# Performance work log

Hardware: AMD Instinct MI355X
Metric: run time of the kernel (lower is better)

The kernel has to match this reference:

```python
import jax, jax.numpy as jnp
import numpy as np
import math

FEAT_DIM = 256
QUERY_DIM = 256
HIDDEN = 64
OUT_DIM = 256
HEADS = 8


def setup_inputs() -> dict:
    key = jax.random.key(0)
    ks = jax.random.split(key, 10)
    B, NQ, NKV = 2, 2048, 2048
    s_q = 1.0 / math.sqrt(QUERY_DIM)
    s_f = 1.0 / math.sqrt(FEAT_DIM)
    s_o = 1.0 / math.sqrt(HIDDEN * HEADS)
    return {
        "feat": jax.random.normal(ks[0], (B, NKV, FEAT_DIM), jnp.float32),
        "query": jax.random.normal(ks[1], (B, NQ, QUERY_DIM), jnp.float32),
        # stacked per-head weights (each head has its own Linear in torch)
        "Wq": jax.random.uniform(ks[2], (HEADS, QUERY_DIM, HIDDEN), jnp.float32, -s_q, s_q),
        "bq": jax.random.uniform(ks[3], (HEADS, HIDDEN), jnp.float32, -s_q, s_q),
        "Wk": jax.random.uniform(ks[4], (HEADS, FEAT_DIM, HIDDEN), jnp.float32, -s_f, s_f),
        "bk": jax.random.uniform(ks[5], (HEADS, HIDDEN), jnp.float32, -s_f, s_f),
        "Wv": jax.random.uniform(ks[6], (HEADS, FEAT_DIM, HIDDEN), jnp.float32, -s_f, s_f),
        "bv": jax.random.uniform(ks[7], (HEADS, HIDDEN), jnp.float32, -s_f, s_f),
        "Wo": jax.random.uniform(ks[8], (HEADS * HIDDEN, OUT_DIM), jnp.float32, -s_o, s_o),
        "bo": jax.random.uniform(ks[9], (OUT_DIM,), jnp.float32, -s_o, s_o),
    }


def reference(feat, query, Wq, bq, Wk, bk, Wv, bv, Wo, bo):
    # Per-head projections, vectorized over the head axis h.
    # q: [B, H, Nq, E]; k, v: [B, H, Nkv, E]
    q = jnp.einsum("bnd,hde->bhne", query, Wq) + bq[None, :, None, :]
    k = jnp.einsum("bnd,hde->bhne", feat, Wk) + bk[None, :, None, :]
    v = jnp.einsum("bnd,hde->bhne", feat, Wv) + bv[None, :, None, :]
    scale = 1.0 / math.sqrt(HIDDEN)
    scores = jnp.einsum("bhqe,bhke->bhqk", q, k) * scale  # [B, H, Nq, Nkv]
    prob = jax.nn.softmax(scores, axis=-1)
    # dropout p=0.0 (eval) -> identity
    heads = jnp.einsum("bhqk,bhke->bhqe", prob, v)  # [B, H, Nq, E]
    # concat heads in order (head 0 first) then output projection
    B, H, NQ, E = heads.shape
    cat = heads.transpose(0, 2, 1, 3).reshape(B, NQ, H * E)
    return cat @ Wo + bo
```

## Files before the change

kernel.cpp:

```cpp
#include <hip/hip_runtime.h>
#include <hip/hip_bf16.h>

typedef unsigned short u16;
typedef __attribute__((ext_vector_type(8))) short short8;
typedef __attribute__((ext_vector_type(4))) float f32x4;
typedef __attribute__((ext_vector_type(16))) float f32x16;
typedef __attribute__((ext_vector_type(2))) int v2i;

#define HEADS 8
#define HID 64
#define QSCALE 0.18033688011112042f

__device__ inline u16 f2bf(float f){
    unsigned u = __float_as_uint(f);
    unsigned r = (u + 0x7fffu + ((u >> 16) & 1u)) >> 16;
    return (u16)r;
}

__device__ inline int cvtpk(float lo, float hi){
    int r;
    asm("v_cvt_pk_bf16_f32 %0, %1, %2" : "=v"(r) : "v"(lo), "v"(hi));
    return r;
}

__device__ inline float exp2fast(float x){
    float r;
    asm("v_exp_f32 %0, %1" : "=v"(r) : "v"(x));
    return r;
}

__device__ inline float xhalf_sum(float x){
    v2i r = __builtin_amdgcn_permlane32_swap(__float_as_int(x), __float_as_int(x), false, false);
    return __int_as_float(r.x) + __int_as_float(r.y);
}

__global__ __launch_bounds__(256) void prep_weights(
    const float* __restrict__ query, const float* __restrict__ feat,
    const float* __restrict__ Wq, const float* __restrict__ Wk,
    const float* __restrict__ Wv, const float* __restrict__ Wo,
    u16* __restrict__ Xbq, u16* __restrict__ Xbf,
    u16* __restrict__ WqT, u16* __restrict__ WkT, u16* __restrict__ WvT,
    u16* __restrict__ WoT)
{
    int id = blockIdx.x * 256 + threadIdx.x;
    if (id < 262144) {
        const float* src = (id < 131072) ? query : feat;
        u16* dst = (id < 131072) ? Xbq : Xbf;
        int r = (id < 131072) ? id : id - 131072;
        float4 a = *reinterpret_cast<const float4*>(&src[r * 8]);
        float4 b = *reinterpret_cast<const float4*>(&src[r * 8 + 4]);
        uint4 s;
        s.x = (unsigned)cvtpk(a.x, a.y);
        s.y = (unsigned)cvtpk(a.z, a.w);
        s.z = (unsigned)cvtpk(b.x, b.y);
        s.w = (unsigned)cvtpk(b.z, b.w);
        *reinterpret_cast<uint4*>(&dst[r * 8]) = s;
    } else if (id < 655360) {
        int id2 = id - 262144;
        int w = id2 / 131072;
        int r = id2 % 131072;
        int c = r >> 8;
        int d = r & 255;
        const float* W = (w == 0) ? Wq : (w == 1 ? Wk : Wv);
        u16* WT = (w == 0) ? WqT : (w == 1 ? WkT : WvT);
        WT[c * 256 + d] = f2bf(W[(c >> 6) * (256 * 64) + d * 64 + (c & 63)]);
    } else {
        int r = id - 655360;
        int o = r >> 9;
        int k = r & 511;
        WoT[o * 512 + k] = f2bf(Wo[k * 256 + o]);
    }
}

__global__ __launch_bounds__(256) void proj_kernel(
    const u16* __restrict__ Xbq, const u16* __restrict__ Xbf,
    const u16* __restrict__ WqT, const u16* __restrict__ WkT, const u16* __restrict__ WvT,
    const float* __restrict__ bq, const float* __restrict__ bk, const float* __restrict__ bv,
    u16* __restrict__ Qb, u16* __restrict__ KVf)
{
    int lb = blockIdx.x;
    int t8 = lb & 7;
    int m = lb >> 3;
    int which = (m < 64) ? 0 : (m < 128 ? 1 : 2);
    int mm = m & 63;
    int m0 = (((t8 >> 2) << 5) | (mm & 31)) * 64;
    int n0 = (((t8 & 3) << 1) | (mm >> 5)) * 64;

    const u16* Xb = (which == 0) ? Xbq : Xbf;
    const u16* WT = (which == 0) ? WqT : (which == 1 ? WkT : WvT);
    const float* bias = (which == 0) ? bq : (which == 1 ? bk : bv);
    int t = threadIdx.x;
    int lane = t & 63, w = t >> 6;
    int l15 = lane & 15, kof = (lane >> 4) * 8;

    __shared__ __align__(16) u16 lA[64][72];
    __shared__ __align__(16) u16 lB[64][72];

    f32x4 acc[4] = {};
    for (int kt = 0; kt < 256; kt += 64) {
        #pragma unroll
        for (int i = 0; i < 2; i++) {
            int lin = t + i * 256;
            int row = lin >> 3, c8 = (lin & 7) * 8;
            *reinterpret_cast<uint4*>(&lA[row][c8]) =
                *reinterpret_cast<const uint4*>(&Xb[(m0 + row) * 256 + kt + c8]);
            *reinterpret_cast<uint4*>(&lB[row][c8]) =
                *reinterpret_cast<const uint4*>(&WT[(n0 + row) * 256 + kt + c8]);
        }
        __syncthreads();
        #pragma unroll
        for (int ks = 0; ks < 2; ks++) {
            short8 a = *reinterpret_cast<const short8*>(&lA[w * 16 + l15][ks * 32 + kof]);
            #pragma unroll
            for (int nt = 0; nt < 4; nt++) {
                short8 b = *reinterpret_cast<const short8*>(&lB[nt * 16 + l15][ks * 32 + kof]);
                acc[nt] = __builtin_amdgcn_mfma_f32_16x16x32_bf16(a, b, acc[nt], 0, 0, 0);
            }
        }
        __syncthreads();
    }
    #pragma unroll
    for (int nt = 0; nt < 4; nt++) {
        #pragma unroll
        for (int i = 0; i < 4; i++) {
            int mrow = m0 + w * 16 + (lane >> 4) * 4 + i;
            int col = n0 + nt * 16 + l15;
            float val = acc[nt][i] + bias[col];
            int b_ = mrow >> 11, n = mrow & 2047;
            int h = col >> 6, e = col & 63;
            int bh = b_ * 8 + h;
            if (which == 0) {
                Qb[(bh * 2048 + n) * 64 + e] = f2bf(val * QSCALE);
            } else {
                int tile = n >> 6, nl = n & 63;
                size_t base = ((size_t)(bh * 32 + tile)) * 8192;
                size_t idx;
                if (which == 1) {
                    int reg  = ((nl >> 5) << 2) | (e >> 4);
                    int ln   = (nl & 31) | (((e >> 3) & 1) << 5);
                    idx = base + reg * 512 + ln * 8 + (e & 7);
                } else {
                    int reg  = ((e >> 5) << 2) | (nl >> 4);
                    int ln   = (e & 31) | (((nl >> 3) & 1) << 5);
                    idx = base + 4096 + reg * 512 + ln * 8 + (nl & 7);
                }
                KVf[idx] = f2bf(val);
            }
        }
    }
}

__global__ __launch_bounds__(512, 2) void attn_kernel(
    const u16* __restrict__ Qb, const u16* __restrict__ KVf, u16* __restrict__ cat)
{
    int lb = blockIdx.x;
    int chunk = lb >> 4;
    int bh = ((lb & 7) << 1) | ((lb >> 3) & 1);
    int b_ = bh >> 3, head = bh & 7;
    int t = threadIdx.x, lane = t & 63, w = t >> 6;
    int l31 = lane & 31, hh = lane >> 5;
    int sp = w >> 1, kvh = w & 1, wi = w >> 1;
    int q0 = chunk * 128 + sp * 32;

    __shared__ __align__(16) u16 smem[34304];
    u16* tiles = smem;
    float* Ol = (float*)smem;
    float* Ll = (float*)((char*)smem + 67584);

    const u16* KVfB = KVf + ((size_t)(bh * 32 + kvh * 16)) * 8192;

    short8 qf[4];
    {
        const u16* qp = Qb + (bh * 2048 + q0 + l31) * 64 + hh * 8;
        #pragma unroll
        for (int kc = 0; kc < 4; kc++)
            qf[kc] = *reinterpret_cast<const short8*>(qp + kc * 16);
    }
    asm volatile("s_waitcnt vmcnt(0)" ::: "memory");

#define PACKP(sb, base, out) {                                              \
        int A0 = cvtpk(sb[base+0], sb[base+1]);                             \
        int B0 = cvtpk(sb[base+4], sb[base+5]);                             \
        v2i r0 = __builtin_amdgcn_permlane32_swap(A0, B0, false, false);    \
        int A1 = cvtpk(sb[base+2], sb[base+3]);                             \
        int B1 = cvtpk(sb[base+6], sb[base+7]);                             \
        v2i r1 = __builtin_amdgcn_permlane32_swap(A1, B1, false, false);    \
        union { int i[4]; short8 s; } uu;                                   \
        uu.i[0] = r0.x; uu.i[1] = r1.x; uu.i[2] = r0.y; uu.i[3] = r1.y;     \
        out = uu.s; }

    auto stage = [&](int buf, int tile) {
        const u16* gsrc = KVfB + (size_t)tile * 8192;
        u16* ldst = tiles + (kvh * 2 + buf) * 8192;
        #pragma unroll
        for (int c = 0; c < 4; c++) {
            int off = (wi * 4 + c) * 512 + lane * 8;
            __builtin_amdgcn_global_load_lds(
                (const __attribute__((address_space(1))) unsigned int*)(const void*)(gsrc + off),
                (__attribute__((address_space(3))) unsigned int*)(void*)(ldst + off),
                16, 0, 0);
        }
    };

    f32x16 o0 = {}, o1 = {};
    float ac0 = 0.f, ac1 = 0.f, ac2 = 0.f, ac3 = 0.f;

    stage(0, 0);
    int cur = 0;
    for (int tt = 0; tt < 16; tt++) {
        if (tt < 15) {
            stage(cur ^ 1, tt + 1);
            asm volatile("s_waitcnt vmcnt(4)" ::: "memory");
        } else {
            asm volatile("s_waitcnt vmcnt(0)" ::: "memory");
        }
        __builtin_amdgcn_s_barrier();
        __builtin_amdgcn_sched_barrier(0);

        const u16* kbase = tiles + (kvh * 2 + cur) * 8192;
        short8 kf[8], vf[8];
        #pragma unroll
        for (int r = 0; r < 8; r++)
            kf[r] = *reinterpret_cast<const short8*>(kbase + r * 512 + lane * 8);
        #pragma unroll
        for (int r = 0; r < 8; r++)
            vf[r] = *reinterpret_cast<const short8*>(kbase + 4096 + r * 512 + lane * 8);

        f32x16 s0 = {}, s1 = {};
        #pragma unroll
        for (int kc = 0; kc < 4; kc++)
            s0 = __builtin_amdgcn_mfma_f32_32x32x16_bf16(kf[kc], qf[kc], s0, 0, 0, 0);
        #pragma unroll
        for (int kc = 0; kc < 4; kc++)
            s1 = __builtin_amdgcn_mfma_f32_32x32x16_bf16(kf[4 + kc], qf[kc], s1, 0, 0, 0);

        #pragma unroll
        for (int r = 0; r < 16; r++) {
            float p0 = exp2fast(s0[r]);
            float p1 = exp2fast(s1[r]);
            s0[r] = p0; s1[r] = p1;
            if ((r & 3) == 0) ac0 += p0 + p1;
            else if ((r & 3) == 1) ac1 += p0 + p1;
            else if ((r & 3) == 2) ac2 += p0 + p1;
            else ac3 += p0 + p1;
        }

        short8 pf[4];
        PACKP(s0, 0, pf[0]); PACKP(s0, 8, pf[1]);
        PACKP(s1, 0, pf[2]); PACKP(s1, 8, pf[3]);

        #pragma unroll
        for (int c = 0; c < 4; c++) {
            o0 = __builtin_amdgcn_mfma_f32_32x32x16_bf16(vf[c],     pf[c], o0, 0, 0, 0);
            o1 = __builtin_amdgcn_mfma_f32_32x32x16_bf16(vf[4 + c], pf[c], o1, 0, 0, 0);
        }

        asm volatile("s_waitcnt lgkmcnt(0)" ::: "memory");
        __builtin_amdgcn_s_barrier();
        __builtin_amdgcn_sched_barrier(0);
        cur ^= 1;
    }

    float lrun = xhalf_sum((ac0 + ac1) + (ac2 + ac3));

    #pragma unroll
    for (int eb = 0; eb < 2; eb++) {
        #pragma unroll
        for (int r = 0; r < 16; r++) {
            int d = eb * 32 + (r & 3) + 8 * (r >> 2) + 4 * hh;
            Ol[(w * 64 + d) * 33 + l31] = eb ? o1[r] : o0[r];
        }
    }
    if (hh == 0) Ll[w * 32 + l31] = lrun;
    __syncthreads();

    {
        int msp = t >> 7;
        int tt2 = t & 127;
        int q = tt2 >> 2;
        int d0 = (tt2 & 3) * 16;
        int wA = msp * 2, wB = msp * 2 + 1;
        float lsum = Ll[wA * 32 + q] + Ll[wB * 32 + q];
        float linv = 1.0f / lsum;
        float vv[16];
        #pragma unroll
        for (int j = 0; j < 16; j++)
            vv[j] = (Ol[(wA * 64 + d0 + j) * 33 + q] +
                     Ol[(wB * 64 + d0 + j) * 33 + q]) * linv;
        uint4 st0, st1;
        st0.x = (unsigned)cvtpk(vv[0],  vv[1]);
        st0.y = (unsigned)cvtpk(vv[2],  vv[3]);
        st0.z = (unsigned)cvtpk(vv[4],  vv[5]);
        st0.w = (unsigned)cvtpk(vv[6],  vv[7]);
        st1.x = (unsigned)cvtpk(vv[8],  vv[9]);
        st1.y = (unsigned)cvtpk(vv[10], vv[11]);
        st1.z = (unsigned)cvtpk(vv[12], vv[13]);
        st1.w = (unsigned)cvtpk(vv[14], vv[15]);
        u16* crow = cat + (b_ * 2048 + chunk * 128 + msp * 32 + q) * 512 + head * 64 + d0;
        *reinterpret_cast<uint4*>(crow) = st0;
        *reinterpret_cast<uint4*>(crow + 8) = st1;
    }
#undef PACKP
}

__global__ __launch_bounds__(256) void outproj_kernel(
    const u16* __restrict__ cat, const u16* __restrict__ WoT,
    const float* __restrict__ bo, float* __restrict__ out)
{
    int m0 = blockIdx.x * 64, n0 = blockIdx.y * 64;
    int t = threadIdx.x, lane = t & 63, w = t >> 6;
    int l15 = lane & 15, kof = (lane >> 4) * 8;

    __shared__ __align__(16) u16 lA[64][72];
    __shared__ __align__(16) u16 lB[64][72];

    f32x4 acc[4] = {};
    for (int kt = 0; kt < 512; kt += 64) {
        #pragma unroll
        for (int i = 0; i < 2; i++) {
            int lin = t + i * 256;
            int row = lin >> 3, c8 = (lin & 7) * 8;
            *reinterpret_cast<uint4*>(&lA[row][c8]) =
                *reinterpret_cast<const uint4*>(&cat[(m0 + row) * 512 + kt + c8]);
            *reinterpret_cast<uint4*>(&lB[row][c8]) =
                *reinterpret_cast<const uint4*>(&WoT[(n0 + row) * 512 + kt + c8]);
        }
        __syncthreads();
        #pragma unroll
        for (int ks = 0; ks < 2; ks++) {
            short8 a = *reinterpret_cast<const short8*>(&lA[w * 16 + l15][ks * 32 + kof]);
            #pragma unroll
            for (int nt = 0; nt < 4; nt++) {
                short8 b = *reinterpret_cast<const short8*>(&lB[nt * 16 + l15][ks * 32 + kof]);
                acc[nt] = __builtin_amdgcn_mfma_f32_16x16x32_bf16(a, b, acc[nt], 0, 0, 0);
            }
        }
        __syncthreads();
    }
    #pragma unroll
    for (int i = 0; i < 4; i++) {
        int mrow = m0 + w * 16 + (lane >> 4) * 4 + i;
        #pragma unroll
        for (int nt = 0; nt < 4; nt++) {
            int col = n0 + nt * 16 + l15;
            out[mrow * 256 + col] = acc[nt][i] + bo[col];
        }
    }
}

extern "C" void kernel_launch(void* const* d_in, const int* in_sizes, int n_in,
                              void* d_out, int out_size, void* d_ws, size_t ws_size,
                              hipStream_t stream) {
    const float* feat  = (const float*)d_in[0];
    const float* query = (const float*)d_in[1];
    const float* Wq = (const float*)d_in[2];
    const float* bq = (const float*)d_in[3];
    const float* Wk = (const float*)d_in[4];
    const float* bk = (const float*)d_in[5];
    const float* Wv = (const float*)d_in[6];
    const float* bv = (const float*)d_in[7];
    const float* Wo = (const float*)d_in[8];
    const float* bo = (const float*)d_in[9];
    float* out = (float*)d_out;

    char* ws = (char*)d_ws;
    u16* WqT = (u16*)(ws + 0);
    u16* WkT = (u16*)(ws + 262144);
    u16* WvT = (u16*)(ws + 524288);
    u16* WoT = (u16*)(ws + 786432);
    u16* Qb  = (u16*)(ws + 1048576);
    u16* KVf = (u16*)(ws + 5242880);
    u16* cat = (u16*)(ws + 13631488);
    u16* Xbq = (u16*)(ws + 17825792);
    u16* Xbf = (u16*)(ws + 19922944);

    hipLaunchKernelGGL(prep_weights, dim3(3072), dim3(256), 0, stream,
                       query, feat, Wq, Wk, Wv, Wo, Xbq, Xbf, WqT, WkT, WvT, WoT);
    hipLaunchKernelGGL(proj_kernel, dim3(1536), dim3(256), 0, stream,
                       Xbq, Xbf, WqT, WkT, WvT, bq, bk, bv, Qb, KVf);
    hipLaunchKernelGGL(attn_kernel, dim3(256), dim3(512), 0, stream,
                       Qb, KVf, cat);
    hipLaunchKernelGGL(outproj_kernel, dim3(64, 4), dim3(256), 0, stream,
                       cat, WoT, bo, out);
}
```

Measured before the change: 52.51 us.

## Pre-swizzle projection operands into MFMA fragment layout and use 32x32 MFMA

After: 51.22 us (median of 2 runs). -2.5%, faster.

```diff
diff --git a/kernel.cpp b/kernel.cpp
--- a/kernel.cpp
+++ b/kernel.cpp
@@ -39,14 +39,16 @@
     const float* __restrict__ Wq, const float* __restrict__ Wk,
     const float* __restrict__ Wv, const float* __restrict__ Wo,
     u16* __restrict__ Xbq, u16* __restrict__ Xbf,
-    u16* __restrict__ WqT, u16* __restrict__ WkT, u16* __restrict__ WvT,
-    u16* __restrict__ WoT)
+    u16* __restrict__ WfT, u16* __restrict__ WoT)
 {
     int id = blockIdx.x * 256 + threadIdx.x;
     if (id < 262144) {
         const float* src = (id < 131072) ? query : feat;
         u16* dst = (id < 131072) ? Xbq : Xbf;
         int r = (id < 131072) ? id : id - 131072;
+        int row = r >> 5;
+        int rb = row >> 5, r5 = row & 31;
+        int ks = (r & 31) >> 1, hi = r & 1;
         float4 a = *reinterpret_cast<const float4*>(&src[r * 8]);
         float4 b = *reinterpret_cast<const float4*>(&src[r * 8 + 4]);
         uint4 s;
@@ -54,7 +56,7 @@
         s.y = (unsigned)cvtpk(a.z, a.w);
         s.z = (unsigned)cvtpk(b.x, b.y);
         s.w = (unsigned)cvtpk(b.z, b.w);
-        *reinterpret_cast<uint4*>(&dst[r * 8]) = s;
+        *reinterpret_cast<uint4*>(&dst[((rb * 16 + ks) * 64 + hi * 32 + r5) * 8]) = s;
     } else if (id < 655360) {
         int id2 = id - 262144;
         int w = id2 / 131072;
@@ -62,8 +64,9 @@
         int c = r >> 8;
         int d = r & 255;
         const float* W = (w == 0) ? Wq : (w == 1 ? Wk : Wv);
-        u16* WT = (w == 0) ? WqT : (w == 1 ? WkT : WvT);
-        WT[c * 256 + d] = f2bf(W[(c >> 6) * (256 * 64) + d * 64 + (c & 63)]);
+        size_t idx = (size_t)(((w * 16 + (c >> 5)) * 16 + (d >> 4)) * 64
+                              + ((d >> 3) & 1) * 32 + (c & 31)) * 8 + (d & 7);
+        WfT[idx] = f2bf(W[(c >> 6) * (256 * 64) + d * 64 + (c & 63)]);
     } else {
         int r = id - 655360;
         int o = r >> 9;
@@ -72,79 +75,113 @@
     }
 }
 
-__global__ __launch_bounds__(256) void proj_kernel(
+__global__ __launch_bounds__(256, 2) void proj_kernel(
     const u16* __restrict__ Xbq, const u16* __restrict__ Xbf,
-    const u16* __restrict__ WqT, const u16* __restrict__ WkT, const u16* __restrict__ WvT,
+    const u16* __restrict__ WfT,
     const float* __restrict__ bq, const float* __restrict__ bk, const float* __restrict__ bv,
     u16* __restrict__ Qb, u16* __restrict__ KVf)
 {
     int lb = blockIdx.x;
-    int t8 = lb & 7;
-    int m = lb >> 3;
-    int which = (m < 64) ? 0 : (m < 128 ? 1 : 2);
-    int mm = m & 63;
-    int m0 = (((t8 >> 2) << 5) | (mm & 31)) * 64;
-    int n0 = (((t8 & 3) << 1) | (mm >> 5)) * 64;
-
+    int which = lb % 3;
+    int rem = lb / 3;
+    int rb = rem & 127;
+    int nh = rem >> 7;
     const u16* Xb = (which == 0) ? Xbq : Xbf;
-    const u16* WT = (which == 0) ? WqT : (which == 1 ? WkT : WvT);
     const float* bias = (which == 0) ? bq : (which == 1 ? bk : bv);
-    int t = threadIdx.x;
-    int lane = t & 63, w = t >> 6;
-    int l15 = lane & 15, kof = (lane >> 4) * 8;
-
-    __shared__ __align__(16) u16 lA[64][72];
-    __shared__ __align__(16) u16 lB[64][72];
-
-    f32x4 acc[4] = {};
-    for (int kt = 0; kt < 256; kt += 64) {
-        #pragma unroll
-        for (int i = 0; i < 2; i++) {
-            int lin = t + i * 256;
-            int row = lin >> 3, c8 = (lin & 7) * 8;
-            *reinterpret_cast<uint4*>(&lA[row][c8]) =
-                *reinterpret_cast<const uint4*>(&Xb[(m0 + row) * 256 + kt + c8]);
-            *reinterpret_cast<uint4*>(&lB[row][c8]) =
-                *reinterpret_cast<const uint4*>(&WT[(n0 + row) * 256 + kt + c8]);
-        }
-        __syncthreads();
-        #pragma unroll
-        for (int ks = 0; ks < 2; ks++) {
-            short8 a = *reinterpret_cast<const short8*>(&lA[w * 16 + l15][ks * 32 + kof]);
+
+    int t = threadIdx.x, lane = t & 63, w = t >> 6;
+    int l31 = lane & 31, hh = lane >> 5;
+
+    __shared__ __align__(16) u16 Xl[8192];
+
+    {
+        const u16* gsrc = Xb + (size_t)rb * 8192;
+        #pragma unroll
+        for (int c = 0; c < 4; c++) {
+            int off = (w * 4 + c) * 512 + lane * 8;
+            __builtin_amdgcn_global_load_lds(
+                (const __attribute__((address_space(1))) unsigned int*)(const void*)(gsrc + off),
+                (__attribute__((address_space(3))) unsigned int*)(void*)(Xl + off),
+                16, 0, 0);
+        }
+    }
+    asm volatile("s_waitcnt vmcnt(0)" ::: "memory");
+    __syncthreads();
+
+    int nb0 = nh * 8 + w * 2;
+    const u16* W0 = WfT + (size_t)(which * 16 + nb0) * 8192 + lane * 8;
+    const u16* W1 = W0 + 8192;
+
+    f32x16 acc0 = {}, acc1 = {};
+    #pragma unroll
+    for (int ks = 0; ks < 16; ks++) {
+        short8 xf = *reinterpret_cast<const short8*>(Xl + ks * 512 + lane * 8);
+        short8 w0 = *reinterpret_cast<const short8*>(W0 + ks * 512);
+        short8 w1 = *reinterpret_cast<const short8*>(W1 + ks * 512);
+        if (which == 2) {
+            acc0 = __builtin_amdgcn_mfma_f32_32x32x16_bf16(xf, w0, acc0, 0, 0, 0);
+            acc1 = __builtin_amdgcn_mfma_f32_32x32x16_bf16(xf, w1, acc1, 0, 0, 0);
+        } else {
+            acc0 = __builtin_amdgcn_mfma_f32_32x32x16_bf16(w0, xf, acc0, 0, 0, 0);
+            acc1 = __builtin_amdgcn_mfma_f32_32x32x16_bf16(w1, xf, acc1, 0, 0, 0);
+        }
+    }
+
+    int h = nh * 4 + w;
+    int nbase = nh * 256 + w * 64;
+
+    if (which != 2) {
+        int m = rb * 32 + l31;
+        int b_ = m >> 11, nq = m & 2047;
+        int bh = b_ * 8 + h;
+        int tile = nq >> 6, nl = nq & 63;
+        #pragma unroll
+        for (int f = 0; f < 2; f++) {
+            const f32x16& A = f ? acc1 : acc0;
             #pragma unroll
-            for (int nt = 0; nt < 4; nt++) {
-                short8 b = *reinterpret_cast<const short8*>(&lB[nt * 16 + l15][ks * 32 + kof]);
-                acc[nt] = __builtin_amdgcn_mfma_f32_16x16x32_bf16(a, b, acc[nt], 0, 0, 0);
+            for (int g = 0; g < 4; g++) {
+                int e0 = f * 32 + g * 8 + 4 * hh;
+                float4 b4 = *reinterpret_cast<const float4*>(&bias[nbase + e0]);
+                float v0 = A[4*g+0] + b4.x, v1 = A[4*g+1] + b4.y;
+                float v2 = A[4*g+2] + b4.z, v3 = A[4*g+3] + b4.w;
+                v2i st;
+                if (which == 0) {
+                    st.x = cvtpk(v0 * QSCALE, v1 * QSCALE);
+                    st.y = cvtpk(v2 * QSCALE, v3 * QSCALE);
+                    *reinterpret_cast<v2i*>(&Qb[(size_t)(bh * 2048 + nq) * 64 + e0]) = st;
+                } else {
+                    st.x = cvtpk(v0, v1);
+                    st.y = cvtpk(v2, v3);
+                    int regK = ((nl >> 5) << 2) | (e0 >> 4);
+                    int lnK  = (nl & 31) | (((e0 >> 3) & 1) << 5);
+                    size_t idx = (size_t)(bh * 32 + tile) * 8192 + regK * 512 + lnK * 8 + (e0 & 7);
+                    *reinterpret_cast<v2i*>(&KVf[idx]) = st;
+                }
             }
         }
-        __syncthreads();
-    }
-    #pragma unroll
-    for (int nt = 0; nt < 4; nt++) {
-        #pragma unroll
-        for (int i = 0; i < 4; i++) {
-            int mrow = m0 + w * 16 + (lane >> 4) * 4 + i;
-            int col = n0 + nt * 16 + l15;
-            float val = acc[nt][i] + bias[col];
-            int b_ = mrow >> 11, n = mrow & 2047;
-            int h = col >> 6, e = col & 63;
-            int bh = b_ * 8 + h;
-            if (which == 0) {
-                Qb[(bh * 2048 + n) * 64 + e] = f2bf(val * QSCALE);
-            } else {
-                int tile = n >> 6, nl = n & 63;
-                size_t base = ((size_t)(bh * 32 + tile)) * 8192;
-                size_t idx;
-                if (which == 1) {
-                    int reg  = ((nl >> 5) << 2) | (e >> 4);
-                    int ln   = (nl & 31) | (((e >> 3) & 1) << 5);
-                    idx = base + reg * 512 + ln * 8 + (e & 7);
-                } else {
-                    int reg  = ((e >> 5) << 2) | (nl >> 4);
-                    int ln   = (e & 31) | (((nl >> 3) & 1) << 5);
-                    idx = base + 4096 + reg * 512 + ln * 8 + (nl & 7);
-                }
-                KVf[idx] = f2bf(val);
+    } else {
+        #pragma unroll
+        for (int f = 0; f < 2; f++) {
+            const f32x16& A = f ? acc1 : acc0;
+            int n_g = nbase + f * 32 + l31;
+            int e = n_g & 63;
+            float bscal = bias[n_g];
+            #pragma unroll
+            for (int g = 0; g < 4; g++) {
+                int kvl = g * 8 + 4 * hh;
+                int m = rb * 32 + kvl;
+                int b_ = m >> 11, nkv = m & 2047;
+                int tile = nkv >> 6, nl = nkv & 63;
+                int bh = b_ * 8 + h;
+                float v0 = A[4*g+0] + bscal, v1 = A[4*g+1] + bscal;
+                float v2 = A[4*g+2] + bscal, v3 = A[4*g+3] + bscal;
+                v2i st;
+                st.x = cvtpk(v0, v1);
+                st.y = cvtpk(v2, v3);
+                int regV = ((e >> 5) << 2) | (nl >> 4);
+                int lnV  = (e & 31) | (((nl >> 3) & 1) << 5);
+                size_t idx = (size_t)(bh * 32 + tile) * 8192 + 4096 + regV * 512 + lnV * 8 + (nl & 7);
+                *reinterpret_cast<v2i*>(&KVf[idx]) = st;
             }
         }
     }
@@ -364,9 +401,7 @@
     float* out = (float*)d_out;
 
     char* ws = (char*)d_ws;
-    u16* WqT = (u16*)(ws + 0);
-    u16* WkT = (u16*)(ws + 262144);
-    u16* WvT = (u16*)(ws + 524288);
+    u16* WfT = (u16*)(ws + 0);
     u16* WoT = (u16*)(ws + 786432);
     u16* Qb  = (u16*)(ws + 1048576);
     u16* KVf = (u16*)(ws + 5242880);
@@ -375,9 +410,9 @@
     u16* Xbf = (u16*)(ws + 19922944);
 
     hipLaunchKernelGGL(prep_weights, dim3(3072), dim3(256), 0, stream,
-                       query, feat, Wq, Wk, Wv, Wo, Xbq, Xbf, WqT, WkT, WvT, WoT);
-    hipLaunchKernelGGL(proj_kernel, dim3(1536), dim3(256), 0, stream,
-                       Xbq, Xbf, WqT, WkT, WvT, bq, bk, bv, Qb, KVf);
+                       query, feat, Wq, Wk, Wv, Wo, Xbq, Xbf, WfT, WoT);
+    hipLaunchKernelGGL(proj_kernel, dim3(768), dim3(256), 0, stream,
+                       Xbq, Xbf, WfT, bq, bk, bv, Qb, KVf);
     hipLaunchKernelGGL(attn_kernel, dim3(256), dim3(512), 0, stream,
                        Qb, KVf, cat);
     hipLaunchKernelGGL(outproj_kernel, dim3(64, 4), dim3(256), 0, stream,
```
